# Performance work log

Measured on AMD Instinct MI355X. Metric: run time of the kernel, lower is better.

The kernel has to match this reference:

```python
import jax, jax.numpy as jnp
import numpy as np

N_MED = 100000   # len(medicine_it): nodes in the single hyperedge
VOCAB = 200000   # medicine vocab (rows of both embedding tables)
C_IN = 256
C_OUT = 256


def setup_inputs() -> dict:
    key = jax.random.key(0)
    k1, k2, k3, k4, k5 = jax.random.split(key, 5)
    return {
        "medicine_it": jax.random.randint(k1, (N_MED,), 0, VOCAB),
        "m_embeddings": jax.random.normal(k2, (VOCAB, C_IN), dtype=jnp.float32),
        "pretrained_weight": jax.random.normal(k3, (VOCAB, C_OUT), dtype=jnp.float32),
        "W": jax.random.normal(k4, (C_OUT, C_IN), dtype=jnp.float32) / np.sqrt(C_IN).astype(np.float32),
        "bias": jax.random.normal(k5, (C_OUT,), dtype=jnp.float32) * 0.01,
    }


def reference(medicine_it, m_embeddings, pretrained_weight, W, bias):
    # --- forward(): gather medicine rows, HypergraphConv with ONE hyperedge ---
    x = m_embeddings[medicine_it]                 # [N, C_in]  row gather
    xw = x @ W.T                                  # [N, C_out] lin (bias added after propagation, as in PyG)
    n = xw.shape[0]
    # Single hyperedge containing all N nodes: edge degree B = N, node degree D = 1.
    # edge_feat = B^{-1} H^T (X W^T);  node_out = D^{-1} H edge_feat + bias (same for all nodes)
    edge_feat = jnp.sum(xw, axis=0) / jnp.asarray(n, xw.dtype)   # [C_out]
    med_node_feature = edge_feat[None, :] + bias                 # [1, C_out], identical per node
    # --- output(): sum_i pretrained[m_i] + sum_i representation[i] ---
    embedding_pretrained = jnp.sum(pretrained_weight[medicine_it], axis=0, keepdims=True)  # [1, C_out]
    embedding_trained = jnp.asarray(n, xw.dtype) * med_node_feature                        # [1, C_out]
    return (embedding_pretrained + embedding_trained)[None, :, :]  # [1, 1, C_out]
```

## Files before the change

### kernel.cpp

```cpp
#include <hip/hip_runtime.h>


__global__ __launch_bounds__(256) void gather_sum_kernel(
    const int* __restrict__ idx,
    const float* __restrict__ memb,
    const float* __restrict__ pre,
    float* __restrict__ gS,
    float* __restrict__ gP,
    int n)
{
    const int lane = threadIdx.x & 63;
    const int wave = threadIdx.x >> 6;
    const int globalWave = blockIdx.x * 4 + wave;
    const int totalWaves = gridDim.x * 4;

    float4 accS = make_float4(0.f, 0.f, 0.f, 0.f);
    float4 accP = make_float4(0.f, 0.f, 0.f, 0.f);

    for (int i = globalWave; i < n; i += totalWaves) {
        const int r = idx[i];
        const float4* mrow = reinterpret_cast<const float4*>(memb + (size_t)r * 256);
        const float4* prow = reinterpret_cast<const float4*>(pre  + (size_t)r * 256);
        const float4 a = mrow[lane];
        const float4 b = prow[lane];
        accS.x += a.x; accS.y += a.y; accS.z += a.z; accS.w += a.w;
        accP.x += b.x; accP.y += b.y; accP.z += b.z; accP.w += b.w;
    }

    __shared__ float sS[256];
    __shared__ float sP[256];
    sS[threadIdx.x] = 0.f;
    sP[threadIdx.x] = 0.f;
    __syncthreads();

    const int c = lane * 4;
    atomicAdd(&sS[c + 0], accS.x);
    atomicAdd(&sS[c + 1], accS.y);
    atomicAdd(&sS[c + 2], accS.z);
    atomicAdd(&sS[c + 3], accS.w);
    atomicAdd(&sP[c + 0], accP.x);
    atomicAdd(&sP[c + 1], accP.y);
    atomicAdd(&sP[c + 2], accP.z);
    atomicAdd(&sP[c + 3], accP.w);
    __syncthreads();

    atomicAdd(&gS[threadIdx.x], sS[threadIdx.x]);
    atomicAdd(&gP[threadIdx.x], sP[threadIdx.x]);
}

__global__ __launch_bounds__(256) void finish_kernel(
    const float* __restrict__ gS,
    const float* __restrict__ gP,
    const float* __restrict__ W,
    const float* __restrict__ bias,
    float* __restrict__ out,
    float nf)
{
    const int c = blockIdx.x;
    const int t = threadIdx.x;

    float v = W[(size_t)c * 256 + t] * gS[t];

    for (int off = 32; off > 0; off >>= 1)
        v += __shfl_down(v, off, 64);

    __shared__ float part[4];
    if ((t & 63) == 0) part[t >> 6] = v;
    __syncthreads();

    if (t == 0) {
        const float s = part[0] + part[1] + part[2] + part[3];
        out[c] = s + gP[c] + nf * bias[c];
    }
}

extern "C" void kernel_launch(void* const* d_in, const int* in_sizes, int n_in,
                              void* d_out, int out_size, void* d_ws, size_t ws_size,
                              hipStream_t stream)
{
    const int*   idx  = (const int*)d_in[0];
    const float* memb = (const float*)d_in[1];
    const float* pre  = (const float*)d_in[2];
    const float* W    = (const float*)d_in[3];
    const float* bias = (const float*)d_in[4];
    float* out = (float*)d_out;

    const int n = in_sizes[0];

    float* gS = (float*)d_ws;
    float* gP = gS + 256;

    hipMemsetAsync(d_ws, 0, 512 * sizeof(float), stream);

    gather_sum_kernel<<<512, 256, 0, stream>>>(idx, memb, pre, gS, gP, n);
    finish_kernel<<<256, 256, 0, stream>>>(gS, gP, W, bias, out, (float)n);
}
```

Baseline: 57.65 us.

## Chunk indices per wave with shuffle broadcast, enlarge grid, replicate accumulators

Each wave now takes a contiguous chunk of indices, loads them in one coalesced read and broadcasts each with a shuffle. The grid grows fourfold so more gathers are in flight to hide memory latency. Global atomics are spread over eight accumulator copies, which the finish kernel sums, to cut contention. In exchange there are more blocks and atomics overall and a slightly larger memset.

```diff
diff --git a/kernel.cpp b/kernel.cpp
--- a/kernel.cpp
+++ b/kernel.cpp
@@ -1,28 +1,34 @@
 #include <hip/hip_runtime.h>
 
+
+#define NCOPY 8
+#define GRID_GATHER 2048
 
 __global__ __launch_bounds__(256) void gather_sum_kernel(
     const int* __restrict__ idx,
     const float* __restrict__ memb,
     const float* __restrict__ pre,
-    float* __restrict__ gS,
-    float* __restrict__ gP,
+    float* __restrict__ acc,
     int n)
 {
     const int lane = threadIdx.x & 63;
-    const int wave = threadIdx.x >> 6;
-    const int globalWave = blockIdx.x * 4 + wave;
-    const int totalWaves = gridDim.x * 4;
+    const int wid  = (blockIdx.x * blockDim.x + threadIdx.x) >> 6;
+    const int nwaves = (GRID_GATHER * 256) >> 6;
+
+    const int per   = (n + nwaves - 1) / nwaves;
+    const int start = wid * per;
+    const int cnt   = min(per, n - start);
+
+    int myidx = 0;
+    if (lane < cnt) myidx = idx[start + lane];
 
     float4 accS = make_float4(0.f, 0.f, 0.f, 0.f);
     float4 accP = make_float4(0.f, 0.f, 0.f, 0.f);
 
-    for (int i = globalWave; i < n; i += totalWaves) {
-        const int r = idx[i];
-        const float4* mrow = reinterpret_cast<const float4*>(memb + (size_t)r * 256);
-        const float4* prow = reinterpret_cast<const float4*>(pre  + (size_t)r * 256);
-        const float4 a = mrow[lane];
-        const float4 b = prow[lane];
+    for (int k = 0; k < cnt; ++k) {
+        const int r = __shfl(myidx, k, 64);
+        const float4 a = reinterpret_cast<const float4*>(memb + (size_t)r * 256)[lane];
+        const float4 b = reinterpret_cast<const float4*>(pre  + (size_t)r * 256)[lane];
         accS.x += a.x; accS.y += a.y; accS.z += a.z; accS.w += a.w;
         accP.x += b.x; accP.y += b.y; accP.z += b.z; accP.w += b.w;
     }
@@ -44,13 +50,13 @@
     atomicAdd(&sP[c + 3], accP.w);
     __syncthreads();
 
-    atomicAdd(&gS[threadIdx.x], sS[threadIdx.x]);
-    atomicAdd(&gP[threadIdx.x], sP[threadIdx.x]);
+    float* myacc = acc + (size_t)(blockIdx.x & (NCOPY - 1)) * 512;
+    atomicAdd(&myacc[threadIdx.x],       sS[threadIdx.x]);
+    atomicAdd(&myacc[256 + threadIdx.x], sP[threadIdx.x]);
 }
 
 __global__ __launch_bounds__(256) void finish_kernel(
-    const float* __restrict__ gS,
-    const float* __restrict__ gP,
+    const float* __restrict__ acc,
     const float* __restrict__ W,
     const float* __restrict__ bias,
     float* __restrict__ out,
@@ -59,7 +65,11 @@
     const int c = blockIdx.x;
     const int t = threadIdx.x;
 
-    float v = W[(size_t)c * 256 + t] * gS[t];
+    float s_t = 0.f;
+    #pragma unroll
+    for (int cp = 0; cp < NCOPY; ++cp) s_t += acc[cp * 512 + t];
+
+    float v = W[(size_t)c * 256 + t] * s_t;
 
     for (int off = 32; off > 0; off >>= 1)
         v += __shfl_down(v, off, 64);
@@ -69,8 +79,10 @@
     __syncthreads();
 
     if (t == 0) {
-        const float s = part[0] + part[1] + part[2] + part[3];
-        out[c] = s + gP[c] + nf * bias[c];
+        float p_c = 0.f;
+        #pragma unroll
+        for (int cp = 0; cp < NCOPY; ++cp) p_c += acc[cp * 512 + 256 + c];
+        out[c] = (part[0] + part[1] + part[2] + part[3]) + p_c + nf * bias[c];
     }
 }
 
@@ -87,11 +99,10 @@
 
     const int n = in_sizes[0];
 
-    float* gS = (float*)d_ws;
-    float* gP = gS + 256;
+    float* acc = (float*)d_ws;
 
-    hipMemsetAsync(d_ws, 0, 512 * sizeof(float), stream);
+    hipMemsetAsync(d_ws, 0, NCOPY * 512 * sizeof(float), stream);
 
-    gather_sum_kernel<<<512, 256, 0, stream>>>(idx, memb, pre, gS, gP, n);
-    finish_kernel<<<256, 256, 0, stream>>>(gS, gP, W, bias, out, (float)n);
+    gather_sum_kernel<<<GRID_GATHER, 256, 0, stream>>>(idx, memb, pre, acc, n);
+    finish_kernel<<<256, 256, 0, stream>>>(acc, W, bias, out, (float)n);
 }
```

Result: slower. 62.64 us (+8.7%).
